# Kernel tuning notes

Hardware: AMD Instinct MI355X
Metric: run time of the kernel (lower is better)

## Reference

```python
import jax, jax.numpy as jnp
import numpy as np

N_HEADS = 8


def setup_inputs() -> dict:
    key = jax.random.key(0)
    k1, k2, k3, k4, k5 = jax.random.split(key, 5)
    B, C, H, W = 32, 64, 64, 64   # z; S = H*W = 4096 = l_h*l_h
    S = H * W
    z = jax.random.normal(k1, (B, C, H, W), dtype=jnp.float32)
    x = jax.random.normal(k2, (B, 64, 64, 64), dtype=jnp.float32)  # c1 must be 64 (input_dim_1)
    # torch.nn.Linear weights: [out_features, in_features], bias=False
    W_Q = jax.random.normal(k3, (S, S), dtype=jnp.float32) * (1.0 / np.sqrt(S)).astype(np.float32)
    W_K = jax.random.normal(k4, (S, S), dtype=jnp.float32) * (1.0 / np.sqrt(S)).astype(np.float32)
    W_V = jax.random.normal(k5, (64, 64), dtype=jnp.float32) * 0.125
    return {"z": z, "x": x, "W_Q": W_Q, "W_K": W_K, "W_V": W_V}


def reference(z, x, W_Q, W_K, W_V):
    n_heads = N_HEADS
    B, C, H, W = z.shape
    S = H * W
    d_k = S // n_heads
    b1, c1, h1, w1 = x.shape
    S1 = h1 * w1

    a = z.reshape(B, C, S)                       # b c (h w)
    r = x.reshape(b1, c1, S1).transpose(0, 2, 1)  # b (h w) c

    # torch Linear: y = x @ W.T; then raw reshapes exactly as in the source
    Q = jnp.einsum('bcs,ts->bct', a, W_Q).reshape(n_heads * B, d_k, C)
    K = jnp.einsum('bcs,ts->bct', a, W_K).reshape(n_heads * B, d_k, C)
    V = jnp.einsum('bsc,tc->bst', r, W_V).reshape(n_heads * b1, S1 // n_heads, C)

    # scores = Q^T K / sqrt(d_k): [nB, C, C]
    scores = jnp.einsum('ndc,nde->nce', Q, K) / jnp.float32(np.sqrt(d_k))
    attn = jax.nn.softmax(scores, axis=-1)

    # context = LeakyReLU(V @ attn, 0.2): [nB, S1//n_heads, C]
    context = jax.nn.leaky_relu(jnp.matmul(V, attn), negative_slope=0.2)
    context = context.transpose(0, 2, 1)          # [nB, C, S1//n_heads]
    return context.reshape(b1, c1, h1, w1)
```

## Files before the change

### kernel.cpp

```cpp
#include <hip/hip_runtime.h>
#include <hip/hip_bf16.h>
#include <stdint.h>

typedef __attribute__((ext_vector_type(8))) __bf16 bf16x8;
typedef __attribute__((ext_vector_type(4))) float f32x4;

#define GLOAD_LDS16(gp, lp) __builtin_amdgcn_global_load_lds( \
    (const __attribute__((address_space(1))) void*)(gp),      \
    (__attribute__((address_space(3))) void*)(lp), 16, 0, 0)

__device__ __forceinline__ uint16_t f2bf_rne(float f) {
  uint32_t u = __float_as_uint(f);
  u += 0x7FFFu + ((u >> 16) & 1u);
  return (uint16_t)(u >> 16);
}

__global__ __launch_bounds__(256) void cvt_z(
    const float* __restrict__ src, uint16_t* __restrict__ dst) {
  int i = blockIdx.x * 256 + threadIdx.x;
  const float4* s4 = (const float4*)src;
  float4 a = s4[2 * i], b = s4[2 * i + 1];
  union { uint16_t u[8]; uint4 v; } o;
  o.u[0] = f2bf_rne(a.x); o.u[1] = f2bf_rne(a.y);
  o.u[2] = f2bf_rne(a.z); o.u[3] = f2bf_rne(a.w);
  o.u[4] = f2bf_rne(b.x); o.u[5] = f2bf_rne(b.y);
  o.u[6] = f2bf_rne(b.z); o.u[7] = f2bf_rne(b.w);
  ((uint4*)dst)[i] = o.v;
}

#define PH_BAR() do { asm volatile("" ::: "memory");            \
                      __builtin_amdgcn_s_barrier();             \
                      asm volatile("" ::: "memory"); } while (0)

#define PACK_B(KT, PB)                                                         \
  do {                                                                         \
    uint4 w0_, w1_;                                                            \
    w0_.x = (uint32_t)f2bf_rne(PB[0][0]) | ((uint32_t)f2bf_rne(PB[0][1]) << 16); \
    w0_.y = (uint32_t)f2bf_rne(PB[0][2]) | ((uint32_t)f2bf_rne(PB[0][3]) << 16); \
    w0_.z = (uint32_t)f2bf_rne(PB[1][0]) | ((uint32_t)f2bf_rne(PB[1][1]) << 16); \
    w0_.w = (uint32_t)f2bf_rne(PB[1][2]) | ((uint32_t)f2bf_rne(PB[1][3]) << 16); \
    w1_.x = (uint32_t)f2bf_rne(PB[2][0]) | ((uint32_t)f2bf_rne(PB[2][1]) << 16); \
    w1_.y = (uint32_t)f2bf_rne(PB[2][2]) | ((uint32_t)f2bf_rne(PB[2][3]) << 16); \
    w1_.z = (uint32_t)f2bf_rne(PB[3][0]) | ((uint32_t)f2bf_rne(PB[3][1]) << 16); \
    w1_.w = (uint32_t)f2bf_rne(PB[3][2]) | ((uint32_t)f2bf_rne(PB[3][3]) << 16); \
    char* Bd_ = lds + (((KT) + 1) & 3) * 32768 + 16384;                        \
    *(uint4*)(Bd_ + bw0) = w0_;                                                \
    *(uint4*)(Bd_ + bw1) = w1_;                                                \
  } while (0)

#define STEP(KT, PB, LB, DO_LD, DO_PK, VMN)                                    \
  do {                                                                         \
    const char* Sb_ = lds + ((KT) & 3) * 32768;                                \
    bf16x8 aa[8], bb[4];                                                       \
    _Pragma("unroll")                                                          \
    for (int n_ = 0; n_ < 4; ++n_)                                             \
      bb[n_] = *(const bf16x8*)(Sb_ + 16384 + boff + n_ * 1024);               \
    _Pragma("unroll")                                                          \
    for (int m_ = 0; m_ < 8; ++m_)                                             \
      aa[m_] = *(const bf16x8*)(Sb_ + aoff + m_ * 1024);                       \
    if (DO_LD) {                                                               \
      _Pragma("unroll")                                                        \
      for (int q_ = 0; q_ < 4; ++q_)                                           \
        LB[q_] = *(const f32x4*)(bsrc + (size_t)((KT) + 3) * 32 + q_ * 4);     \
      GLOAD_LDS16(aptr  + (size_t)((KT) + 3) * 32,                             \
                  lds + (((KT) + 3) & 3) * 32768 + t16);                       \
      GLOAD_LDS16(aptr2 + (size_t)((KT) + 3) * 32,                             \
                  lds + (((KT) + 3) & 3) * 32768 + 8192 + t16);                \
    }                                                                          \
    __builtin_amdgcn_s_setprio(1);                                             \
    _Pragma("unroll")                                                          \
    for (int m_ = 0; m_ < 8; ++m_)                                             \
      _Pragma("unroll")                                                        \
      for (int n_ = 0; n_ < 4; ++n_)                                           \
        acc[m_][n_] = __builtin_amdgcn_mfma_f32_16x16x32_bf16(                 \
            aa[m_], bb[n_], acc[m_][n_], 0, 0, 0);                             \
    __builtin_amdgcn_s_setprio(0);                                             \
    asm volatile("s_waitcnt vmcnt(" #VMN ")" ::: "memory");                    \
    if (DO_PK) PACK_B(KT, PB);                                                 \
    asm volatile("s_waitcnt lgkmcnt(0)" ::: "memory");                         \
    PH_BAR();                                                                  \
  } while (0)

__global__ __launch_bounds__(512, 2) void gemm_qk8wf(
    const uint16_t* __restrict__ A,
    const float* __restrict__ Wq, const float* __restrict__ Wk,
    uint16_t* __restrict__ Cq, uint16_t* __restrict__ Ck) {
  extern __shared__ char lds[];

  const int gid = blockIdx.x;
  const int xcd = gid & 7;
  const int idx = gid >> 3;
  const int which = idx & 1;
  const int r = idx >> 1;
  const int tm = (xcd & 1) * 4 + (r & 3);
  const int tn = (xcd >> 1) * 4 + (r >> 2);

  const float* Bmat = which ? Wk : Wq;
  uint16_t* C = which ? Ck : Cq;
  const int m0 = tm * 256, n0 = tn * 256;

  const int t = threadIdx.x;
  const int lane = t & 63;
  const int w = t >> 6;
  const int wm = w >> 2, wn = w & 3;
  const int t16 = t * 16;

  const int gsw = (((t & 3) ^ ((t >> 3) & 3)) * 8);
  const uint16_t* aptr  = A + (size_t)(m0 + (t >> 2)) * 4096 + gsw;
  const uint16_t* aptr2 = aptr + (size_t)128 * 4096;

  const float* bsrc = Bmat + (size_t)(n0 + (t >> 1)) * 4096 + (t & 1) * 16;
  {
  }
  const int br_ = t >> 1, bh_ = t & 1, bs_ = (br_ >> 1) & 3;
  const int bw0 = br_ * 64 + ((2 * bh_) ^ bs_) * 16;
  const int bw1 = br_ * 64 + ((2 * bh_ + 1) ^ bs_) * 16;

  const int sl = ((lane >> 4) ^ ((lane & 15) >> 1)) & 3;
  const int aoff = (wm * 128 + (lane & 15)) * 64 + sl * 16;
  const int boff = (wn * 64 + (lane & 15)) * 64 + sl * 16;

  f32x4 acc[8][4] = {};
  f32x4 b0[4], b1[4], b2[4];

#pragma unroll
  for (int p = 0; p < 3; ++p) {
    GLOAD_LDS16(aptr  + (size_t)p * 32, lds + p * 32768 + t16);
    GLOAD_LDS16(aptr2 + (size_t)p * 32, lds + p * 32768 + 8192 + t16);
  }
#pragma unroll
  for (int q_ = 0; q_ < 4; ++q_) {
    b0[q_] = *(const f32x4*)(bsrc + q_ * 4);
    b1[q_] = *(const f32x4*)(bsrc + 32 + q_ * 4);
    b2[q_] = *(const f32x4*)(bsrc + 64 + q_ * 4);
  }
  asm volatile("s_waitcnt vmcnt(0)" ::: "memory");
  PACK_B(-1, b0);
  asm volatile("s_waitcnt lgkmcnt(0)" ::: "memory");
  PH_BAR();

  for (int it = 0; it < 41; ++it) {
    const int kt0 = it * 3;
    STEP(kt0 + 0, b1, b0, 1, 1, 12);
    STEP(kt0 + 1, b2, b1, 1, 1, 12);
    STEP(kt0 + 2, b0, b2, 1, 1, 12);
  }
  STEP(123, b1, b0, 1, 1, 12);
  STEP(124, b2, b1, 1, 1, 12);
  STEP(125, b0, b2, 0, 1, 6);
  STEP(126, b1, b2, 0, 1, 0);
  {
    const char* Sb_ = lds + 3 * 32768;
    bf16x8 aa[8], bb[4];
#pragma unroll
    for (int n_ = 0; n_ < 4; ++n_)
      bb[n_] = *(const bf16x8*)(Sb_ + 16384 + boff + n_ * 1024);
#pragma unroll
    for (int m_ = 0; m_ < 8; ++m_)
      aa[m_] = *(const bf16x8*)(Sb_ + aoff + m_ * 1024);
#pragma unroll
    for (int m_ = 0; m_ < 8; ++m_)
#pragma unroll
      for (int n_ = 0; n_ < 4; ++n_)
        acc[m_][n_] = __builtin_amdgcn_mfma_f32_16x16x32_bf16(
            aa[m_], bb[n_], acc[m_][n_], 0, 0, 0);
  }

  const int colb = n0 + wn * 64 + (lane & 15);
  const int rowb = m0 + wm * 128 + (lane >> 4) * 4;
#pragma unroll
  for (int m_ = 0; m_ < 8; ++m_)
#pragma unroll
    for (int n_ = 0; n_ < 4; ++n_)
#pragma unroll
      for (int j = 0; j < 4; ++j)
        C[(size_t)(rowb + m_ * 16 + j) * 4096 + colb + n_ * 16] =
            f2bf_rne(acc[m_][n_][j]);
}

__device__ __forceinline__ bf16x8 load_frag_rot(const uint16_t* buf,
                                                int ij, int thb) {
  union { uint16_t u[8]; bf16x8 v; } r;
#pragma unroll
  for (int e = 0; e < 8; ++e) {
    const int th = thb + e;
    const int rot = (th + 2 * (th >> 3)) & 7;
    const int irot = (ij + rot * 8) & 63;
    r.u[e] = buf[th * 64 + irot];
  }
  return r.v;
}

__global__ __launch_bounds__(256) void attn_scores_mfma(
    const uint16_t* __restrict__ Qb, const uint16_t* __restrict__ Kb,
    float* __restrict__ attn) {
  const int n = blockIdx.x;
  __shared__ uint16_t q_l[2][4096];
  __shared__ uint16_t k_l[2][4096];
  __shared__ float scores_l[64 * 68];

  const int t = threadIdx.x;
  const int lane = t & 63;
  const int w = t >> 6;
  const int i0w = (w >> 1) * 32, j0w = (w & 1) * 32;

  const uint16_t* Qn = Qb + (size_t)n * 32768;
  const uint16_t* Kn = Kb + (size_t)n * 32768;

  const int g1 = t, g2 = t + 256;
  const int th1 = g1 >> 3, th2 = g2 >> 3;
  const int s1 = (((g1 & 7) - ((th1 + 2 * (th1 >> 3)) & 7)) & 7);
  const int s2 = (((g2 & 7) - ((th2 + 2 * (th2 >> 3)) & 7)) & 7);
  const size_t so1 = (size_t)th1 * 64 + s1 * 8;
  const size_t so2 = (size_t)th2 * 64 + s2 * 8;

#define STAGE_CH(bf, cm)                                                    \
  do {                                                                      \
    const size_t co_ = (size_t)(cm) * 4096;                                 \
    GLOAD_LDS16(Qn + co_ + so1, (char*)&q_l[bf][0] + g1 * 16);              \
    GLOAD_LDS16(Qn + co_ + so2, (char*)&q_l[bf][0] + g2 * 16);              \
    GLOAD_LDS16(Kn + co_ + so1, (char*)&k_l[bf][0] + g1 * 16);              \
    GLOAD_LDS16(Kn + co_ + so2, (char*)&k_l[bf][0] + g2 * 16);              \
  } while (0)

  f32x4 acc[2][2] = {};

  STAGE_CH(0, 0);
  asm volatile("s_waitcnt vmcnt(0)" ::: "memory");
  __syncthreads();

  for (int cm = 0; cm < 8; ++cm) {
    const int bf = cm & 1;
    if (cm < 7) STAGE_CH(bf ^ 1, cm + 1);
#pragma unroll
    for (int ks = 0; ks < 2; ++ks) {
      const int thb = ks * 32 + (lane >> 4) * 8;
      bf16x8 aa0 = load_frag_rot(&q_l[bf][0], i0w + (lane & 15), thb);
      bf16x8 aa1 = load_frag_rot(&q_l[bf][0], i0w + 16 + (lane & 15), thb);
      bf16x8 bb0 = load_frag_rot(&k_l[bf][0], j0w + (lane & 15), thb);
      bf16x8 bb1 = load_frag_rot(&k_l[bf][0], j0w + 16 + (lane & 15), thb);
      acc[0][0] = __builtin_amdgcn_mfma_f32_16x16x32_bf16(aa0, bb0, acc[0][0], 0, 0, 0);
      acc[0][1] = __builtin_amdgcn_mfma_f32_16x16x32_bf16(aa0, bb1, acc[0][1], 0, 0, 0);
      acc[1][0] = __builtin_amdgcn_mfma_f32_16x16x32_bf16(aa1, bb0, acc[1][0], 0, 0, 0);
      acc[1][1] = __builtin_amdgcn_mfma_f32_16x16x32_bf16(aa1, bb1, acc[1][1], 0, 0, 0);
    }
    asm volatile("s_waitcnt vmcnt(0)" ::: "memory");
    __syncthreads();
  }
#undef STAGE_CH

#pragma unroll
  for (int fi = 0; fi < 2; ++fi)
#pragma unroll
    for (int fj = 0; fj < 2; ++fj)
#pragma unroll
      for (int jr = 0; jr < 4; ++jr) {
        const int i = i0w + fi * 16 + (lane >> 4) * 4 + jr;
        const int j = j0w + fj * 16 + (lane & 15);
        scores_l[i * 68 + j] = acc[fi][fj][jr];
      }
  __syncthreads();

  {
    const int i = t >> 2, jg = t & 3;
    float pv[16];
    *(float4*)(pv + 0)  = *(const float4*)&scores_l[i * 68 + jg * 16 + 0];
    *(float4*)(pv + 4)  = *(const float4*)&scores_l[i * 68 + jg * 16 + 4];
    *(float4*)(pv + 8)  = *(const float4*)&scores_l[i * 68 + jg * 16 + 8];
    *(float4*)(pv + 12) = *(const float4*)&scores_l[i * 68 + jg * 16 + 12];
    float m = pv[0];
#pragma unroll
    for (int q = 1; q < 16; ++q) m = fmaxf(m, pv[q]);
    m = fmaxf(m, __shfl_xor(m, 1, 64));
    m = fmaxf(m, __shfl_xor(m, 2, 64));
    const float sc = 0.044194173824159216f * 1.4426950408889634f;
    float e[16];
    float ssum = 0.f;
#pragma unroll
    for (int q = 0; q < 16; ++q) {
      e[q] = exp2f((pv[q] - m) * sc);
      ssum += e[q];
    }
    ssum += __shfl_xor(ssum, 1, 64);
    ssum += __shfl_xor(ssum, 2, 64);
    const float inv = 1.0f / ssum;
    float ov[16];
#pragma unroll
    for (int q = 0; q < 16; ++q) ov[q] = e[q] * inv;
    float* dst = attn + (size_t)n * 4096 + i * 64 + jg * 16;
    *(float4*)(dst + 0)  = *(float4*)(ov + 0);
    *(float4*)(dst + 4)  = *(float4*)(ov + 4);
    *(float4*)(dst + 8)  = *(float4*)(ov + 8);
    *(float4*)(dst + 12) = *(float4*)(ov + 12);
  }
}

__global__ __launch_bounds__(256) void ctx_kernel(
    const float* __restrict__ x, const float* __restrict__ Wv,
    const float* __restrict__ attn, float* __restrict__ out) {
  const int n = blockIdx.x >> 3, ut = blockIdx.x & 7;
  const int b = n >> 3, g = n & 7;
  const int u0 = ut * 64;
  __shared__ float attn_l[64 * 64];
  __shared__ float wv_l[64 * 64];
  __shared__ float x_l[64 * 64];
  __shared__ float v_l[64 * 64];
  const int t = threadIdx.x;

#pragma unroll
  for (int r = 0; r < 4; ++r) {
    ((float4*)attn_l)[r * 256 + t] =
        ((const float4*)(attn + (size_t)n * 4096))[r * 256 + t];
    ((float4*)wv_l)[r * 256 + t] = ((const float4*)Wv)[r * 256 + t];
  }
  {
    const float* xbase = x + (size_t)b * 262144 + (size_t)g * 512 + u0;
    const int ul4 = (t & 15) * 4;
    const int cc0 = t >> 4;
#pragma unroll
    for (int r = 0; r < 4; ++r) {
      int cc = cc0 + r * 16;
      *(float4*)&x_l[cc * 64 + ul4] = *(const float4*)&xbase[(size_t)cc * 4096 + ul4];
    }
  }
  __syncthreads();
  {
    const int ul = t & 63, e0 = t >> 6;
    float vacc[16];
#pragma unroll
    for (int ee = 0; ee < 16; ++ee) vacc[ee] = 0.f;
    for (int cc = 0; cc < 64; ++cc) {
      float xv = x_l[cc * 64 + ul];
#pragma unroll
      for (int ee = 0; ee < 16; ++ee)
        vacc[ee] += xv * wv_l[(e0 + 4 * ee) * 64 + cc];
    }
#pragma unroll
    for (int ee = 0; ee < 16; ++ee) v_l[(e0 + 4 * ee) * 64 + ul] = vacc[ee];
  }
  __syncthreads();
  {
    const int ul = t & 63, j0 = t >> 6;
    float cacc[16];
#pragma unroll
    for (int jj = 0; jj < 16; ++jj) cacc[jj] = 0.f;
    for (int c = 0; c < 64; ++c) {
      float vv = v_l[c * 64 + ul];
#pragma unroll
      for (int jj = 0; jj < 16; ++jj)
        cacc[jj] += vv * attn_l[c * 64 + j0 + 4 * jj];
    }
    float* ob = out + (size_t)b * 262144 + (size_t)g * 8 * 4096;
#pragma unroll
    for (int jj = 0; jj < 16; ++jj) {
      int j = j0 + 4 * jj;
      float v = cacc[jj];
      v = v > 0.f ? v : 0.2f * v;
      ob[(size_t)(j >> 3) * 4096 + (size_t)(j & 7) * 512 + u0 + ul] = v;
    }
  }
}

extern "C" void kernel_launch(void* const* d_in, const int* in_sizes, int n_in,
                              void* d_out, int out_size, void* d_ws, size_t ws_size,
                              hipStream_t stream) {
  const float* z  = (const float*)d_in[0];
  const float* x  = (const float*)d_in[1];
  const float* Wq = (const float*)d_in[2];
  const float* Wk = (const float*)d_in[3];
  const float* Wv = (const float*)d_in[4];
  float* out = (float*)d_out;

  char* ws = (char*)d_ws;
  uint16_t* zb   = (uint16_t*)(ws);
  uint16_t* qbo  = (uint16_t*)(ws + 16777216);
  uint16_t* kbo  = (uint16_t*)(ws + 33554432);
  float*    attn = (float*)(ws + 50331648);

  cvt_z<<<4096, 256, 0, stream>>>(z, zb);

  (void)hipFuncSetAttribute((const void*)gemm_qk8wf,
                            hipFuncAttributeMaxDynamicSharedMemorySize, 131072);
  gemm_qk8wf<<<256, 512, 131072, stream>>>(zb, Wq, Wk, qbo, kbo);

  attn_scores_mfma<<<256, 256, 0, stream>>>(qbo, kbo, attn);
  ctx_kernel<<<2048, 256, 0, stream>>>(x, Wv, attn, out);
}
```

Measured before the change: 229.5 us.

## Restructure QK GEMM to K=64 steps with double-buffered LDS and padded B layout

The QK projection GEMM now consumes 64 K-elements per pipeline step instead of 32, moving from a 4-slot ring with 3-deep prefetch to a two-slot double buffer. The A tile uses an 8-way XOR swizzle and the bf16-converted B tile uses a padded row stride of 144 bytes. This halves the number of barriers and loop iterations, amortising synchronisation and issue overhead over more MFMAs per step. In exchange it uses more LDS (139264 bytes) and keeps only one step of prefetch in flight, which may expose more global-load latency.

```diff
diff --git a/kernel.cpp b/kernel.cpp
--- a/kernel.cpp
+++ b/kernel.cpp
@@ -28,44 +28,46 @@
   ((uint4*)dst)[i] = o.v;
 }
 
+#define SLOT 69632
 #define PH_BAR() do { asm volatile("" ::: "memory");            \
                       __builtin_amdgcn_s_barrier();             \
                       asm volatile("" ::: "memory"); } while (0)
 
-#define PACK_B(KT, PB)                                                         \
+#define PACK_B(SS)                                                             \
   do {                                                                         \
-    uint4 w0_, w1_;                                                            \
-    w0_.x = (uint32_t)f2bf_rne(PB[0][0]) | ((uint32_t)f2bf_rne(PB[0][1]) << 16); \
-    w0_.y = (uint32_t)f2bf_rne(PB[0][2]) | ((uint32_t)f2bf_rne(PB[0][3]) << 16); \
-    w0_.z = (uint32_t)f2bf_rne(PB[1][0]) | ((uint32_t)f2bf_rne(PB[1][1]) << 16); \
-    w0_.w = (uint32_t)f2bf_rne(PB[1][2]) | ((uint32_t)f2bf_rne(PB[1][3]) << 16); \
-    w1_.x = (uint32_t)f2bf_rne(PB[2][0]) | ((uint32_t)f2bf_rne(PB[2][1]) << 16); \
-    w1_.y = (uint32_t)f2bf_rne(PB[2][2]) | ((uint32_t)f2bf_rne(PB[2][3]) << 16); \
-    w1_.z = (uint32_t)f2bf_rne(PB[3][0]) | ((uint32_t)f2bf_rne(PB[3][1]) << 16); \
-    w1_.w = (uint32_t)f2bf_rne(PB[3][2]) | ((uint32_t)f2bf_rne(PB[3][3]) << 16); \
-    char* Bd_ = lds + (((KT) + 1) & 3) * 32768 + 16384;                        \
-    *(uint4*)(Bd_ + bw0) = w0_;                                                \
-    *(uint4*)(Bd_ + bw1) = w1_;                                                \
+    _Pragma("unroll")                                                          \
+    for (int q_ = 0; q_ < 4; ++q_) {                                           \
+      uint4 wv_;                                                               \
+      wv_.x = (uint32_t)f2bf_rne(bld[2*q_][0]) |                               \
+              ((uint32_t)f2bf_rne(bld[2*q_][1]) << 16);                        \
+      wv_.y = (uint32_t)f2bf_rne(bld[2*q_][2]) |                               \
+              ((uint32_t)f2bf_rne(bld[2*q_][3]) << 16);                        \
+      wv_.z = (uint32_t)f2bf_rne(bld[2*q_+1][0]) |                             \
+              ((uint32_t)f2bf_rne(bld[2*q_+1][1]) << 16);                      \
+      wv_.w = (uint32_t)f2bf_rne(bld[2*q_+1][2]) |                             \
+              ((uint32_t)f2bf_rne(bld[2*q_+1][3]) << 16);                      \
+      *(uint4*)(lds + (SS) + 32768 + bwo + q_ * 16) = wv_;                     \
+    }                                                                          \
   } while (0)
 
-#define STEP(KT, PB, LB, DO_LD, DO_PK, VMN)                                    \
+#define STEP(KT, SB, SS, DO_LD)                                                \
   do {                                                                         \
-    const char* Sb_ = lds + ((KT) & 3) * 32768;                                \
+    const char* Ab_ = lds + (SB);                                              \
     bf16x8 aa[8], bb[4];                                                       \
     _Pragma("unroll")                                                          \
     for (int n_ = 0; n_ < 4; ++n_)                                             \
-      bb[n_] = *(const bf16x8*)(Sb_ + 16384 + boff + n_ * 1024);               \
+      bb[n_] = *(const bf16x8*)(Ab_ + boff0 + n_ * 2304);                      \
     _Pragma("unroll")                                                          \
     for (int m_ = 0; m_ < 8; ++m_)                                             \
-      aa[m_] = *(const bf16x8*)(Sb_ + aoff + m_ * 1024);                       \
+      aa[m_] = *(const bf16x8*)(Ab_ + aoff0 + m_ * 2048);                      \
     if (DO_LD) {                                                               \
       _Pragma("unroll")                                                        \
-      for (int q_ = 0; q_ < 4; ++q_)                                           \
-        LB[q_] = *(const f32x4*)(bsrc + (size_t)((KT) + 3) * 32 + q_ * 4);     \
-      GLOAD_LDS16(aptr  + (size_t)((KT) + 3) * 32,                             \
-                  lds + (((KT) + 3) & 3) * 32768 + t16);                       \
-      GLOAD_LDS16(aptr2 + (size_t)((KT) + 3) * 32,                             \
-                  lds + (((KT) + 3) & 3) * 32768 + 8192 + t16);                \
+      for (int q_ = 0; q_ < 8; ++q_)                                           \
+        bld[q_] = *(const f32x4*)(bsrc + (size_t)((KT) + 1) * 64 + q_ * 4);    \
+      _Pragma("unroll")                                                        \
+      for (int i_ = 0; i_ < 4; ++i_)                                           \
+        GLOAD_LDS16(aptr + (size_t)i_ * 64 * 4096 + (size_t)((KT) + 1) * 64,   \
+                    lds + (SS) + i_ * 8192 + t16);                             \
     }                                                                          \
     __builtin_amdgcn_s_setprio(1);                                             \
     _Pragma("unroll")                                                          \
@@ -75,13 +77,30 @@
         acc[m_][n_] = __builtin_amdgcn_mfma_f32_16x16x32_bf16(                 \
             aa[m_], bb[n_], acc[m_][n_], 0, 0, 0);                             \
     __builtin_amdgcn_s_setprio(0);                                             \
-    asm volatile("s_waitcnt vmcnt(" #VMN ")" ::: "memory");                    \
-    if (DO_PK) PACK_B(KT, PB);                                                 \
+    _Pragma("unroll")                                                          \
+    for (int n_ = 0; n_ < 4; ++n_)                                             \
+      bb[n_] = *(const bf16x8*)(Ab_ + boff1 + n_ * 2304);                      \
+    _Pragma("unroll")                                                          \
+    for (int m_ = 0; m_ < 8; ++m_)                                             \
+      aa[m_] = *(const bf16x8*)(Ab_ + aoff1 + m_ * 2048);                      \
+    __builtin_amdgcn_s_setprio(1);                                             \
+    _Pragma("unroll")                                                          \
+    for (int m_ = 0; m_ < 8; ++m_)                                             \
+      _Pragma("unroll")                                                        \
+      for (int n_ = 0; n_ < 4; ++n_)                                           \
+        acc[m_][n_] = __builtin_amdgcn_mfma_f32_16x16x32_bf16(                 \
+            aa[m_], bb[n_], acc[m_][n_], 0, 0, 0);                             \
+    __builtin_amdgcn_s_setprio(0);                                             \
+    if (DO_LD) {                                                               \
+      asm volatile("s_waitcnt vmcnt(4)" ::: "memory");                         \
+      PACK_B(SS);                                                              \
+      asm volatile("s_waitcnt vmcnt(0)" ::: "memory");                         \
+    }                                                                          \
     asm volatile("s_waitcnt lgkmcnt(0)" ::: "memory");                         \
     PH_BAR();                                                                  \
   } while (0)
 
-__global__ __launch_bounds__(512, 2) void gemm_qk8wf(
+__global__ __launch_bounds__(512, 2) void gemm_qk64(
     const uint16_t* __restrict__ A,
     const float* __restrict__ Wq, const float* __restrict__ Wk,
     uint16_t* __restrict__ Cq, uint16_t* __restrict__ Ck) {
@@ -105,66 +124,40 @@
   const int wm = w >> 2, wn = w & 3;
   const int t16 = t * 16;
 
-  const int gsw = (((t & 3) ^ ((t >> 3) & 3)) * 8);
-  const uint16_t* aptr  = A + (size_t)(m0 + (t >> 2)) * 4096 + gsw;
-  const uint16_t* aptr2 = aptr + (size_t)128 * 4096;
-
-  const float* bsrc = Bmat + (size_t)(n0 + (t >> 1)) * 4096 + (t & 1) * 16;
-  {
-  }
-  const int br_ = t >> 1, bh_ = t & 1, bs_ = (br_ >> 1) & 3;
-  const int bw0 = br_ * 64 + ((2 * bh_) ^ bs_) * 16;
-  const int bw1 = br_ * 64 + ((2 * bh_ + 1) ^ bs_) * 16;
-
-  const int sl = ((lane >> 4) ^ ((lane & 15) >> 1)) & 3;
-  const int aoff = (wm * 128 + (lane & 15)) * 64 + sl * 16;
-  const int boff = (wn * 64 + (lane & 15)) * 64 + sl * 16;
+  const int gl_ = (t & 7) ^ ((t >> 3) & 7);
+  const uint16_t* aptr = A + (size_t)(m0 + (t >> 3)) * 4096 + gl_ * 8;
+
+  const float* bsrc = Bmat + (size_t)(n0 + (t >> 1)) * 4096 + (t & 1) * 32;
+  const int bwo = (t >> 1) * 144 + (t & 1) * 64;
+
+  const int arow = wm * 128 + (lane & 15);
+  const int aoff0 = arow * 128 + (((0 * 4 + (lane >> 4)) ^ (lane & 7)) * 16);
+  const int aoff1 = arow * 128 + (((1 * 4 + (lane >> 4)) ^ (lane & 7)) * 16);
+  const int brow = wn * 64 + (lane & 15);
+  const int boff0 = 32768 + brow * 144 + 0 * 64 + (lane >> 4) * 16;
+  const int boff1 = 32768 + brow * 144 + 1 * 64 + (lane >> 4) * 16;
 
   f32x4 acc[8][4] = {};
-  f32x4 b0[4], b1[4], b2[4];
-
-#pragma unroll
-  for (int p = 0; p < 3; ++p) {
-    GLOAD_LDS16(aptr  + (size_t)p * 32, lds + p * 32768 + t16);
-    GLOAD_LDS16(aptr2 + (size_t)p * 32, lds + p * 32768 + 8192 + t16);
-  }
-#pragma unroll
-  for (int q_ = 0; q_ < 4; ++q_) {
-    b0[q_] = *(const f32x4*)(bsrc + q_ * 4);
-    b1[q_] = *(const f32x4*)(bsrc + 32 + q_ * 4);
-    b2[q_] = *(const f32x4*)(bsrc + 64 + q_ * 4);
-  }
-  asm volatile("s_waitcnt vmcnt(0)" ::: "memory");
-  PACK_B(-1, b0);
-  asm volatile("s_waitcnt lgkmcnt(0)" ::: "memory");
+  f32x4 bld[8];
+
+#pragma unroll
+  for (int q_ = 0; q_ < 8; ++q_)
+    bld[q_] = *(const f32x4*)(bsrc + q_ * 4);
+#pragma unroll
+  for (int i_ = 0; i_ < 4; ++i_)
+    GLOAD_LDS16(aptr + (size_t)i_ * 64 * 4096, lds + i_ * 8192 + t16);
+  asm volatile("s_waitcnt vmcnt(4)" ::: "memory");
+  PACK_B(0);
+  asm volatile("s_waitcnt vmcnt(0) lgkmcnt(0)" ::: "memory");
   PH_BAR();
 
-  for (int it = 0; it < 41; ++it) {
-    const int kt0 = it * 3;
-    STEP(kt0 + 0, b1, b0, 1, 1, 12);
-    STEP(kt0 + 1, b2, b1, 1, 1, 12);
-    STEP(kt0 + 2, b0, b2, 1, 1, 12);
-  }
-  STEP(123, b1, b0, 1, 1, 12);
-  STEP(124, b2, b1, 1, 1, 12);
-  STEP(125, b0, b2, 0, 1, 6);
-  STEP(126, b1, b2, 0, 1, 0);
-  {
-    const char* Sb_ = lds + 3 * 32768;
-    bf16x8 aa[8], bb[4];
-#pragma unroll
-    for (int n_ = 0; n_ < 4; ++n_)
-      bb[n_] = *(const bf16x8*)(Sb_ + 16384 + boff + n_ * 1024);
-#pragma unroll
-    for (int m_ = 0; m_ < 8; ++m_)
-      aa[m_] = *(const bf16x8*)(Sb_ + aoff + m_ * 1024);
-#pragma unroll
-    for (int m_ = 0; m_ < 8; ++m_)
-#pragma unroll
-      for (int n_ = 0; n_ < 4; ++n_)
-        acc[m_][n_] = __builtin_amdgcn_mfma_f32_16x16x32_bf16(
-            aa[m_], bb[n_], acc[m_][n_], 0, 0, 0);
-  }
+  for (int it = 0; it < 31; ++it) {
+    const int kt0 = it * 2;
+    STEP(kt0 + 0, 0, SLOT, 1);
+    STEP(kt0 + 1, SLOT, 0, 1);
+  }
+  STEP(62, 0, SLOT, 1);
+  STEP(63, SLOT, 0, 0);
 
   const int colb = n0 + wn * 64 + (lane & 15);
   const int rowb = m0 + wm * 128 + (lane >> 4) * 4;
@@ -379,9 +372,9 @@
 
   cvt_z<<<4096, 256, 0, stream>>>(z, zb);
 
-  (void)hipFuncSetAttribute((const void*)gemm_qk8wf,
-                            hipFuncAttributeMaxDynamicSharedMemorySize, 131072);
-  gemm_qk8wf<<<256, 512, 131072, stream>>>(zb, Wq, Wk, qbo, kbo);
+  (void)hipFuncSetAttribute((const void*)gemm_qk64,
+                            hipFuncAttributeMaxDynamicSharedMemorySize, 139264);
+  gemm_qk64<<<256, 512, 139264, stream>>>(zb, Wq, Wk, qbo, kbo);
 
   attn_scores_mfma<<<256, 256, 0, stream>>>(qbo, kbo, attn);
   ctx_kernel<<<2048, 256, 0, stream>>>(x, Wv, attn, out);
```

Result: slower. 263.3 us (+14.7%).
